# Performance work log

Measured on AMD Instinct MI355X. Metric: run time of the kernel, lower is better.

The kernel has to match this reference:

```python
import jax, jax.numpy as jnp
import numpy as np

B, S, HID = 2, 1024, 2048
N_HEADS, N_KV, HEAD_DIM = 32, 4, 128
BLOCK, MAX_BLOCKS = 32, 128
EPS = 1e-6
ROPE_THETA = 1e6


def _rmsnorm(x, w):
    # per-head RMSNorm over head_dim (Qwen3MoeRMSNorm)
    var = jnp.mean(x * x, axis=-1, keepdims=True)
    return x * jax.lax.rsqrt(var + EPS) * w


def _rotate_half(x):
    h = x.shape[-1] // 2
    return jnp.concatenate([-x[..., h:], x[..., :h]], axis=-1)


def setup_inputs() -> dict:
    key = jax.random.key(0)
    ks = jax.random.split(key, 8)
    hidden_states = jax.random.normal(ks[0], (B, S, HID), dtype=jnp.float32)
    wq = jax.random.normal(ks[1], (N_HEADS * HEAD_DIM, HID), dtype=jnp.float32) * 0.02
    wk = jax.random.normal(ks[2], (N_KV * HEAD_DIM, HID), dtype=jnp.float32) * 0.02
    wv = jax.random.normal(ks[3], (N_KV * HEAD_DIM, HID), dtype=jnp.float32) * 0.02
    wo = jax.random.normal(ks[4], (HID, N_HEADS * HEAD_DIM), dtype=jnp.float32) * 0.02
    q_norm_w = 1.0 + 0.01 * jax.random.normal(ks[5], (HEAD_DIM,), dtype=jnp.float32)
    k_norm_w = 1.0 + 0.01 * jax.random.normal(ks[6], (HEAD_DIM,), dtype=jnp.float32)
    # RoPE tables (rotate-half / llama convention)
    inv_freq = 1.0 / (ROPE_THETA ** (jnp.arange(0, HEAD_DIM, 2, dtype=jnp.float32) / HEAD_DIM))
    t = jnp.arange(S, dtype=jnp.float32)
    freqs = jnp.outer(t, inv_freq)  # [S, HEAD_DIM/2]
    emb = jnp.concatenate([freqs, freqs], axis=-1)  # [S, HEAD_DIM]
    cos, sin = jnp.cos(emb), jnp.sin(emb)
    # page table: B sequences x (S/BLOCK) blocks, distinct block ids
    page_table = jnp.arange(B * (S // BLOCK), dtype=jnp.int32).reshape(B, S // BLOCK)
    return {"hidden_states": hidden_states, "wq": wq, "wk": wk, "wv": wv, "wo": wo,
            "q_norm_w": q_norm_w, "k_norm_w": k_norm_w, "cos": cos, "sin": sin,
            "page_table": page_table}


def reference(hidden_states, wq, wk, wv, wo, q_norm_w, k_norm_w, cos, sin, page_table):
    b, s, _ = hidden_states.shape
    # fused QKV projection (math-equivalent to the concatenated qkv_proj_weight)
    q = (hidden_states @ wq.T).reshape(b, s, N_HEADS, HEAD_DIM)
    k = (hidden_states @ wk.T).reshape(b, s, N_KV, HEAD_DIM)
    v = (hidden_states @ wv.T).reshape(b, s, N_KV, HEAD_DIM)
    # per-head RMSNorm then RoPE
    q = _rmsnorm(q, q_norm_w)
    k = _rmsnorm(k, k_norm_w)
    c = cos[None, :, None, :]
    sn = sin[None, :, None, :]
    q = q * c + _rotate_half(q) * sn
    k = k * c + _rotate_half(k) * sn
    # paged KV-cache fill: [B, nblk, BLOCK, kvh, hd] -> cache[block_id, kvh, BLOCK, hd]
    nblk = s // BLOCK
    k_blk = k.reshape(b, nblk, BLOCK, N_KV, HEAD_DIM).transpose(0, 1, 3, 2, 4).reshape(-1, N_KV, BLOCK, HEAD_DIM)
    v_blk = v.reshape(b, nblk, BLOCK, N_KV, HEAD_DIM).transpose(0, 1, 3, 2, 4).reshape(-1, N_KV, BLOCK, HEAD_DIM)
    flat_pt = page_table.reshape(-1)
    cache_k = jnp.zeros((MAX_BLOCKS, N_KV, BLOCK, HEAD_DIM), dtype=k.dtype).at[flat_pt].set(k_blk)
    cache_v = jnp.zeros((MAX_BLOCKS, N_KV, BLOCK, HEAD_DIM), dtype=v.dtype).at[flat_pt].set(v_blk)
    # GQA: repeat kv heads (num_key_value_groups = 8)
    groups = N_HEADS // N_KV
    k_rep = jnp.repeat(k, groups, axis=2)  # [b, s, N_HEADS, hd]
    v_rep = jnp.repeat(v, groups, axis=2)
    # causal SDPA, scaling = head_dim ** -0.5
    scale = HEAD_DIM ** -0.5
    scores = jnp.einsum('bqhd,bkhd->bhqk', q, k_rep) * scale
    causal = jnp.tril(jnp.ones((s, s), dtype=bool))
    scores = jnp.where(causal[None, None], scores, jnp.finfo(scores.dtype).min)
    probs = jax.nn.softmax(scores, axis=-1)
    attn = jnp.einsum('bhqk,bkhd->bqhd', probs, v_rep).reshape(b, s, N_HEADS * HEAD_DIM)
    out = attn @ wo.T  # [b, s, HID]
    return out, cache_k, cache_v
```

## Files before the change

### kernel.cpp

```cpp
#include <hip/hip_runtime.h>
#include <hip/hip_bf16.h>


typedef __attribute__((ext_vector_type(8))) __bf16 bf16x8;
typedef __attribute__((ext_vector_type(4))) __bf16 bf16x4;
typedef __attribute__((ext_vector_type(4))) float f32x4;

__device__ __forceinline__ void gload16(const void* g, void* l) {
    __builtin_amdgcn_global_load_lds((const __attribute__((address_space(1))) void*)g,
                                     (__attribute__((address_space(3))) void*)l, 16, 0, 0);
}

__global__ __launch_bounds__(256) void cvt5(const float* __restrict__ s0, const float* __restrict__ s1,
                                            const float* __restrict__ s2, const float* __restrict__ s3,
                                            const float* __restrict__ s4,
                                            __bf16* __restrict__ d0, __bf16* __restrict__ d1,
                                            __bf16* __restrict__ d2, __bf16* __restrict__ d3,
                                            __bf16* __restrict__ d4) {
    const int b = blockIdx.x;
    const float* src; __bf16* dst; int off;
    if (b < 4096)       { src = s0; dst = d0; off = b; }
    else if (b < 12288) { src = s1; dst = d1; off = b - 4096; }
    else if (b < 13312) { src = s2; dst = d2; off = b - 12288; }
    else if (b < 14336) { src = s3; dst = d3; off = b - 13312; }
    else                { src = s4; dst = d4; off = b - 14336; }
    const int i = off * 256 + threadIdx.x;
    float4 v = reinterpret_cast<const float4*>(src)[i];
    bf16x4 o = {(__bf16)v.x, (__bf16)v.y, (__bf16)v.z, (__bf16)v.w};
    reinterpret_cast<bf16x4*>(dst)[i] = o;
}

__global__ __launch_bounds__(256) void reduce_add(float* __restrict__ o,
                                                  const float* __restrict__ p, int n4) {
    int i = blockIdx.x * 256 + threadIdx.x;
    int stride = gridDim.x * 256;
    for (; i < n4; i += stride) {
        float4 a = reinterpret_cast<float4*>(o)[i];
        float4 b = reinterpret_cast<const float4*>(p)[i];
        a.x += b.x; a.y += b.y; a.z += b.z; a.w += b.w;
        reinterpret_cast<float4*>(o)[i] = a;
    }
}

__global__ __launch_bounds__(512, 2) void gemm256(const __bf16* __restrict__ A,
                                                  const __bf16* __restrict__ B,
                                                  __bf16* __restrict__ C,
                                                  const int M, const int N, const int K) {
    __shared__ __bf16 Asm[2 * 256 * 64];
    __shared__ __bf16 Bsm[2 * 256 * 64];
    const int tid = threadIdx.x, lane = tid & 63, wave = tid >> 6;
    const int wm = wave >> 2, wn = wave & 3;
    const int lrow = lane & 15, lkg = lane >> 4;
    const int nbn = N >> 8;
    const int swz = ((int)blockIdx.x & 7) * ((int)gridDim.x >> 3) + ((int)blockIdx.x >> 3);
    const int bm = swz / nbn, bn = swz % nbn;
    const int brow = bm * 256, bcol = bn * 256;
    const int row0 = tid >> 3;
    const int scol_sw = ((tid & 7) ^ (row0 & 7)) * 8;
    const __bf16* gA = A + (size_t)(brow + row0) * K + scol_sw;
    const __bf16* gB = B + (size_t)(bcol + row0) * K + scol_sw;
    const int aslot0 = (lkg ^ (lrow & 7)) * 8;
    const int aslot1 = ((4 + lkg) ^ (lrow & 7)) * 8;
    const int nt = K / 64, nIter = nt / 2;

    f32x4 acc[8][4] = {};
    bf16x8 a[4][2];

    auto stage = [&](int s) {
        if (s >= 4 * nt) return;
        const int tau = s >> 2, h = s & 3, hb = s & 1;
        const size_t rofs = (size_t)(hb * 128) * K + (size_t)tau * 64;
        if (h < 2) {
            const __bf16* g = gA + rofs;
            __bf16* l = Asm + (tau & 1) * 16384 + hb * 8192 + tid * 8;
            gload16(g, l);
            gload16(g + (size_t)64 * K, l + 4096);
        } else {
            const __bf16* g = gB + rofs;
            __bf16* l = Bsm + (tau & 1) * 16384 + hb * 8192 + tid * 8;
            gload16(g, l);
            gload16(g + (size_t)64 * K, l + 4096);
        }
    };

    stage(0); stage(1); stage(2); stage(3); stage(4);
    asm volatile("s_waitcnt vmcnt(2)" ::: "memory");
    __builtin_amdgcn_s_barrier();

    for (int i = 0; i < nIter; ++i) {
        const bool last = (i == nIter - 1);
#pragma unroll
        for (int p = 0; p < 8; ++p) {
            const int q = p & 3, cbuf = p >> 2;
            const __bf16* As = Asm + cbuf * 16384;
            const __bf16* Bs = Bsm + cbuf * 16384;
            bf16x8 b[2][2];
            if ((q & 1) == 0) {
#pragma unroll
                for (int mf = 0; mf < 4; ++mf) {
                    const int r = wm * 128 + (q >> 1) * 64 + mf * 16 + lrow;
                    a[mf][0] = *reinterpret_cast<const bf16x8*>(&As[r * 64 + aslot0]);
                    a[mf][1] = *reinterpret_cast<const bf16x8*>(&As[r * 64 + aslot1]);
                }
            }
#pragma unroll
            for (int nf = 0; nf < 2; ++nf) {
                const int r = wn * 64 + (q & 1) * 32 + nf * 16 + lrow;
                b[nf][0] = *reinterpret_cast<const bf16x8*>(&Bs[r * 64 + aslot0]);
                b[nf][1] = *reinterpret_cast<const bf16x8*>(&Bs[r * 64 + aslot1]);
            }
            stage(8 * i + p + 5);
            if (p == 3) {
                if (last) asm volatile("s_waitcnt vmcnt(0)" ::: "memory");
                else      asm volatile("s_waitcnt vmcnt(2)" ::: "memory");
            } else if (p == 7 && !last) {
                asm volatile("s_waitcnt vmcnt(2)" ::: "memory");
            }
            __builtin_amdgcn_s_barrier();
            asm volatile("s_waitcnt lgkmcnt(0)" ::: "memory");
            __builtin_amdgcn_sched_barrier(0);
            __builtin_amdgcn_s_setprio(1);
#pragma unroll
            for (int mf = 0; mf < 4; ++mf)
#pragma unroll
                for (int nf = 0; nf < 2; ++nf)
#pragma unroll
                    for (int kk = 0; kk < 2; ++kk)
                        acc[(q >> 1) * 4 + mf][(q & 1) * 2 + nf] =
                            __builtin_amdgcn_mfma_f32_16x16x32_bf16(
                                a[mf][kk], b[nf][kk],
                                acc[(q >> 1) * 4 + mf][(q & 1) * 2 + nf], 0, 0, 0);
            __builtin_amdgcn_s_setprio(0);
            __builtin_amdgcn_s_barrier();
        }
    }
#pragma unroll
    for (int Mi = 0; Mi < 8; ++Mi)
#pragma unroll
        for (int Ni = 0; Ni < 4; ++Ni)
#pragma unroll
            for (int j = 0; j < 4; ++j) {
                const size_t r = brow + wm * 128 + Mi * 16 + lkg * 4 + j;
                const size_t c = bcol + wn * 64 + Ni * 16 + lrow;
                C[r * N + c] = (__bf16)acc[Mi][Ni][j];
            }
}

template <int OUT_BF16>
__global__ __launch_bounds__(256) void gemm_bt(const __bf16* __restrict__ A,
                                               const __bf16* __restrict__ B,
                                               void* __restrict__ C0,
                                               void* __restrict__ C1,
                                               const int M, const int N, const int K,
                                               const int klen) {
    __shared__ __bf16 As0[128 * 64];
    __shared__ __bf16 Bs0[128 * 64];
    __shared__ __bf16 As1[128 * 64];
    __shared__ __bf16 Bs1[128 * 64];
    const int tid = threadIdx.x;
    const int lane = tid & 63;
    const int wave = tid >> 6;
    const int bn = blockIdx.x, bm = blockIdx.y;
    const int kbeg = blockIdx.z * klen;
    const int brow = bm * 128, bcol = bn * 128;
    const int wr = wave >> 1, wc = wave & 1;
    const int lrow = lane & 15, lkg = lane >> 4;
    const int srow_in = lane >> 3;
    const int scol = (lane & 7) * 8;
    f32x4 acc[4][4] = {};

    auto stage = [&](int k0, __bf16* as, __bf16* bs) {
#pragma unroll
        for (int r = 0; r < 4; ++r) {
            const int chunk = r * 4 + wave;
            const int row = chunk * 8 + srow_in;
            gload16(&A[(size_t)(brow + row) * K + k0 + scol], as + chunk * 512);
            gload16(&B[(size_t)(bcol + row) * K + k0 + scol], bs + chunk * 512);
        }
    };
    auto compute = [&](const __bf16* as, const __bf16* bs) {
#pragma unroll
        for (int kk = 0; kk < 2; ++kk) {
            bf16x8 a[4], bfr[4];
#pragma unroll
            for (int m = 0; m < 4; ++m)
                a[m] = *reinterpret_cast<const bf16x8*>(&as[(wr * 64 + m * 16 + lrow) * 64 + kk * 32 + lkg * 8]);
#pragma unroll
            for (int n = 0; n < 4; ++n)
                bfr[n] = *reinterpret_cast<const bf16x8*>(&bs[(wc * 64 + n * 16 + lrow) * 64 + kk * 32 + lkg * 8]);
#pragma unroll
            for (int m = 0; m < 4; ++m)
#pragma unroll
                for (int n = 0; n < 4; ++n)
                    acc[m][n] = __builtin_amdgcn_mfma_f32_16x16x32_bf16(a[m], bfr[n], acc[m][n], 0, 0, 0);
        }
    };

    const int nt = klen / 64;
    stage(kbeg, As0, Bs0);
    asm volatile("s_waitcnt vmcnt(0)" ::: "memory");
    __syncthreads();
    int t = 0;
    for (; t + 2 < nt; t += 2) {
        stage(kbeg + (t + 1) * 64, As1, Bs1);
        compute(As0, Bs0);
        asm volatile("s_waitcnt vmcnt(0)" ::: "memory");
        __syncthreads();
        stage(kbeg + (t + 2) * 64, As0, Bs0);
        compute(As1, Bs1);
        asm volatile("s_waitcnt vmcnt(0)" ::: "memory");
        __syncthreads();
    }
    stage(kbeg + (t + 1) * 64, As1, Bs1);
    compute(As0, Bs0);
    asm volatile("s_waitcnt vmcnt(0)" ::: "memory");
    __syncthreads();
    compute(As1, Bs1);

    void* C = blockIdx.z == 0 ? C0 : C1;
#pragma unroll
    for (int m = 0; m < 4; ++m)
#pragma unroll
        for (int n = 0; n < 4; ++n)
#pragma unroll
            for (int j = 0; j < 4; ++j) {
                const size_t r = brow + wr * 64 + m * 16 + lkg * 4 + j;
                const size_t c = bcol + wc * 64 + n * 16 + lrow;
                if (OUT_BF16)
                    ((__bf16*)C)[r * N + c] = (__bf16)acc[m][n][j];
                else
                    ((float*)C)[r * N + c] = acc[m][n][j];
            }
}

__global__ __launch_bounds__(256) void norm_rope_cache(
    __bf16* __restrict__ qkv, const float* __restrict__ cosT, const float* __restrict__ sinT,
    const float* __restrict__ qw, const float* __restrict__ kw,
    const int* __restrict__ ptab, float* __restrict__ cacheK, float* __restrict__ cacheV) {
    const int t = blockIdx.x;
    const int b = t >> 10, s = t & 1023;
    const int wave = threadIdx.x >> 6, lane = threadIdx.x & 63;
    __bf16* row = qkv + (size_t)t * 5120;
    const float c = cosT[s * 128 + lane];
    const float sn = sinT[s * 128 + lane];
    const int page = ptab[b * 32 + (s >> 5)];
    const int so = s & 31;
    const float wq0 = qw[lane], wq1 = qw[lane + 64];
#pragma unroll
    for (int i = 0; i < 8; ++i) {
        const int h = wave * 8 + i;
        float x0 = (float)row[h * 128 + lane];
        float x1 = (float)row[h * 128 + 64 + lane];
        float ss = x0 * x0 + x1 * x1;
        for (int off = 32; off; off >>= 1) ss += __shfl_xor(ss, off);
        const float rs = rsqrtf(ss * (1.0f / 128.0f) + 1e-6f);
        const float y0 = x0 * rs * wq0, y1 = x1 * rs * wq1;
        row[h * 128 + lane]      = (__bf16)(y0 * c - y1 * sn);
        row[h * 128 + 64 + lane] = (__bf16)(y1 * c + y0 * sn);
    }
    {
        const int h = wave;
        float x0 = (float)row[4096 + h * 128 + lane];
        float x1 = (float)row[4096 + h * 128 + 64 + lane];
        float ss = x0 * x0 + x1 * x1;
        for (int off = 32; off; off >>= 1) ss += __shfl_xor(ss, off);
        const float rs = rsqrtf(ss * (1.0f / 128.0f) + 1e-6f);
        const float y0 = x0 * rs * kw[lane], y1 = x1 * rs * kw[lane + 64];
        const float o0 = y0 * c - y1 * sn, o1 = y1 * c + y0 * sn;
        row[4096 + h * 128 + lane]      = (__bf16)o0;
        row[4096 + h * 128 + 64 + lane] = (__bf16)o1;
        float* ck = cacheK + (((size_t)page * 4 + h) * 32 + so) * 128;
        ck[lane] = o0; ck[lane + 64] = o1;
        const float v0 = (float)row[4608 + h * 128 + lane];
        const float v1 = (float)row[4608 + h * 128 + 64 + lane];
        float* cv = cacheV + (((size_t)page * 4 + h) * 32 + so) * 128;
        cv[lane] = v0; cv[lane + 64] = v1;
    }
}

__global__ __launch_bounds__(512) void attn_fwd(const __bf16* __restrict__ qkv,
                                                __bf16* __restrict__ out) {
    constexpr int LVT = 72, LPT = 72;
    __shared__ __bf16 Ks[64 * 128];
    __shared__ __bf16 Vt[128 * LVT];
    __shared__ __bf16 Ps[8 * 16 * LPT];
    const int qb = 63 - blockIdx.x;
    const int kvg = blockIdx.y, b = blockIdx.z;
    const int tid = threadIdx.x, wave = tid >> 6, lane = tid & 63;
    const int lrow = lane & 15, lkg = lane >> 4;
    const int h = kvg * 8 + wave;
    const size_t base = (size_t)b * 1024 * 5120;
    const int kofs = 4096 + kvg * 128, vofs = 4608 + kvg * 128;
    const int qrow0 = qb * 16;

    bf16x8 aq[4];
#pragma unroll
    for (int kc = 0; kc < 4; ++kc)
        aq[kc] = *reinterpret_cast<const bf16x8*>(
            &qkv[base + (size_t)(qrow0 + lrow) * 5120 + h * 128 + kc * 32 + lkg * 8]);

    f32x4 acc[8] = {};
    float m_i = -1e30f, l_i = 0.f;
    const int nt = qb / 4 + 1;
    __bf16* Pw = &Ps[wave * 16 * LPT];
    const int swz = lrow & 7;

    for (int t = 0; t < nt; ++t) {
        const int kv0 = t * 64;
        __syncthreads();
#pragma unroll
        for (int c = 0; c < 2; ++c) {
            const int chunk = c * 8 + wave;
            const int row = chunk * 4 + (lane >> 4);
            const int gslot = (lane & 15) ^ (row & 7);
            gload16(&qkv[base + (size_t)(kv0 + row) * 5120 + kofs + gslot * 8],
                    &Ks[chunk * 512]);
        }
#pragma unroll
        for (int r = 0; r < 2; ++r) {
            const int d0 = (wave + r * 8) * 8;
            uint4 vv = *reinterpret_cast<const uint4*>(
                &qkv[base + (size_t)(kv0 + lane) * 5120 + vofs + d0]);
            const __bf16* pv = reinterpret_cast<const __bf16*>(&vv);
#pragma unroll
            for (int j = 0; j < 8; ++j) Vt[(d0 + j) * LVT + lane] = pv[j];
        }
        __syncthreads();

        f32x4 st[4] = {};
#pragma unroll
        for (int kc = 0; kc < 4; ++kc)
#pragma unroll
            for (int f = 0; f < 4; ++f) {
                bf16x8 ak = *reinterpret_cast<const bf16x8*>(
                    &Ks[(f * 16 + lrow) * 128 + ((kc * 4 + lkg) ^ swz) * 8]);
                st[f] = __builtin_amdgcn_mfma_f32_16x16x32_bf16(ak, aq[kc], st[f], 0, 0, 0);
            }

        const int qpos = qrow0 + lrow;
        float sv[16];
        float pmax = -1e30f;
#pragma unroll
        for (int f = 0; f < 4; ++f)
#pragma unroll
            for (int j = 0; j < 4; ++j) {
                const int kvpos = kv0 + f * 16 + lkg * 4 + j;
                float x = st[f][j] * 0.08838834764831845f;
                if (kvpos > qpos) x = -1e30f;
                sv[f * 4 + j] = x;
                pmax = fmaxf(pmax, x);
            }
        pmax = fmaxf(pmax, __shfl_xor(pmax, 16));
        pmax = fmaxf(pmax, __shfl_xor(pmax, 32));
        const float m_new = fmaxf(m_i, pmax);
        const float sf = __expf(m_i - m_new);
        float ladd = 0.f;
#pragma unroll
        for (int f = 0; f < 4; ++f) {
            bf16x4 pb;
#pragma unroll
            for (int j = 0; j < 4; ++j) {
                const float p = __expf(sv[f * 4 + j] - m_new);
                ladd += p;
                pb[j] = (__bf16)p;
            }
            *reinterpret_cast<bf16x4*>(&Pw[lrow * LPT + f * 16 + lkg * 4]) = pb;
        }
        ladd += __shfl_xor(ladd, 16);
        ladd += __shfl_xor(ladd, 32);
        l_i = l_i * sf + ladd;
        m_i = m_new;
        float sfj[4];
#pragma unroll
        for (int j = 0; j < 4; ++j) sfj[j] = __shfl(sf, lkg * 4 + j);
#pragma unroll
        for (int f = 0; f < 8; ++f)
#pragma unroll
            for (int j = 0; j < 4; ++j) acc[f][j] *= sfj[j];

#pragma unroll
        for (int kk = 0; kk < 2; ++kk) {
            bf16x8 ap = *reinterpret_cast<const bf16x8*>(&Pw[lrow * LPT + kk * 32 + lkg * 8]);
#pragma unroll
            for (int f = 0; f < 8; ++f) {
                bf16x8 bv = *reinterpret_cast<const bf16x8*>(
                    &Vt[(f * 16 + lrow) * LVT + kk * 32 + lkg * 8]);
                acc[f] = __builtin_amdgcn_mfma_f32_16x16x32_bf16(ap, bv, acc[f], 0, 0, 0);
            }
        }
    }
    float linv[4];
#pragma unroll
    for (int j = 0; j < 4; ++j) linv[j] = 1.0f / __shfl(l_i, lkg * 4 + j);
#pragma unroll
    for (int f = 0; f < 8; ++f)
#pragma unroll
        for (int j = 0; j < 4; ++j) {
            const size_t r = (size_t)b * 1024 + qrow0 + lkg * 4 + j;
            out[r * 4096 + h * 128 + f * 16 + lrow] = (__bf16)(acc[f][j] * linv[j]);
        }
}

extern "C" void kernel_launch(void* const* d_in, const int* in_sizes, int n_in,
                              void* d_out, int out_size, void* d_ws, size_t ws_size,
                              hipStream_t stream) {
    const float* hidden = (const float*)d_in[0];
    const float* wq = (const float*)d_in[1];
    const float* wk = (const float*)d_in[2];
    const float* wv = (const float*)d_in[3];
    const float* wo = (const float*)d_in[4];
    const float* qnw = (const float*)d_in[5];
    const float* knw = (const float*)d_in[6];
    const float* cosT = (const float*)d_in[7];
    const float* sinT = (const float*)d_in[8];
    const int* ptab = (const int*)d_in[9];

    float* outp = (float*)d_out;
    float* cacheK = outp + 4194304;
    float* cacheV = cacheK + 2097152;

    char* ws = (char*)d_ws;
    __bf16* hbf    = (__bf16*)ws;
    __bf16* w1bf   = (__bf16*)(ws + 8388608);
    __bf16* wobf   = (__bf16*)(ws + 29360128);
    __bf16* qkvbf  = (__bf16*)(ws + 46137344);
    __bf16* attnbf = (__bf16*)ws;
    float*  opart  = (float*)(ws + 46137344);

    cvt5<<<22528, 256, 0, stream>>>(hidden, wq, wk, wv, wo,
                                    hbf, w1bf, w1bf + (size_t)4096 * 2048,
                                    w1bf + (size_t)4608 * 2048, wobf);

    gemm256<<<160, 512, 0, stream>>>(hbf, w1bf, qkvbf, 2048, 5120, 2048);

    hipMemsetAsync(cacheK, 0, (size_t)4194304 * 4, stream);
    norm_rope_cache<<<2048, 256, 0, stream>>>(qkvbf, cosT, sinT, qnw, knw, ptab, cacheK, cacheV);

    attn_fwd<<<dim3(64, 4, 2), 512, 0, stream>>>(qkvbf, attnbf);

    gemm_bt<0><<<dim3(16, 16, 2), 256, 0, stream>>>(attnbf, wobf, outp, opart,
                                                    2048, 2048, 4096, 2048);
    reduce_add<<<2048, 256, 0, stream>>>(outp, opart, 4194304 / 4);
}
```

Baseline: 217.2 us.

## Pair causal query blocks per workgroup and double-buffer K/V in attention

The attention kernel now processes two query blocks per workgroup, a short one and its mirrored long one (qa and 63-qa). This balances causal work across workgroups and halves the grid. K and V tiles are double-buffered, with V prefetched into registers and K staged via async LDS loads one tile ahead. Other changes: the softmax scale is folded into Q, V and P use XOR-swizzled LDS layouts, masking is applied only on the diagonal tile, and the accumulator rescale is skipped when the running max grows by at most 8. Costs are more registers and LDS per workgroup, and skipping the rescale lets unnormalized probabilities reach up to e^8 before the bf16 cast.

```diff
diff --git a/kernel.cpp b/kernel.cpp
--- a/kernel.cpp
+++ b/kernel.cpp
@@ -278,126 +278,187 @@
     }
 }
 
-__global__ __launch_bounds__(512) void attn_fwd(const __bf16* __restrict__ qkv,
-                                                __bf16* __restrict__ out) {
-    constexpr int LVT = 72, LPT = 72;
-    __shared__ __bf16 Ks[64 * 128];
-    __shared__ __bf16 Vt[128 * LVT];
-    __shared__ __bf16 Ps[8 * 16 * LPT];
-    const int qb = 63 - blockIdx.x;
+__global__ __launch_bounds__(512, 2) void attn_fwd(const __bf16* __restrict__ qkv,
+                                                   __bf16* __restrict__ out) {
+    __shared__ __bf16 Ks[2][64 * 128];
+    __shared__ __bf16 Vs[2][128 * 64];
+    __shared__ __bf16 Ps[8][2][16 * 64];
+    const int qa = blockIdx.x;
+    const int qbig = 63 - qa;
     const int kvg = blockIdx.y, b = blockIdx.z;
     const int tid = threadIdx.x, wave = tid >> 6, lane = tid & 63;
     const int lrow = lane & 15, lkg = lane >> 4;
     const int h = kvg * 8 + wave;
     const size_t base = (size_t)b * 1024 * 5120;
     const int kofs = 4096 + kvg * 128, vofs = 4608 + kvg * 128;
-    const int qrow0 = qb * 16;
-
-    bf16x8 aq[4];
-#pragma unroll
-    for (int kc = 0; kc < 4; ++kc)
-        aq[kc] = *reinterpret_cast<const bf16x8*>(
-            &qkv[base + (size_t)(qrow0 + lrow) * 5120 + h * 128 + kc * 32 + lkg * 8]);
-
-    f32x4 acc[8] = {};
-    float m_i = -1e30f, l_i = 0.f;
-    const int nt = qb / 4 + 1;
-    __bf16* Pw = &Ps[wave * 16 * LPT];
-    const int swz = lrow & 7;
-
-    for (int t = 0; t < nt; ++t) {
-        const int kv0 = t * 64;
-        __syncthreads();
+    const int ntA = qa / 4 + 1, nt = qbig / 4 + 1;
+    const int qposA = qa * 16 + lrow, qposB = qbig * 16 + lrow;
+    const int rsw = lrow & 7;
+
+    bf16x8 aqA[4], aqB[4];
+#pragma unroll
+    for (int kc = 0; kc < 4; ++kc) {
+        bf16x8 ta = *reinterpret_cast<const bf16x8*>(
+            &qkv[base + (size_t)(qa * 16 + lrow) * 5120 + h * 128 + kc * 32 + lkg * 8]);
+        bf16x8 tb = *reinterpret_cast<const bf16x8*>(
+            &qkv[base + (size_t)(qbig * 16 + lrow) * 5120 + h * 128 + kc * 32 + lkg * 8]);
+#pragma unroll
+        for (int i = 0; i < 8; ++i) {
+            ta[i] = (__bf16)((float)ta[i] * 0.08838834764831845f);
+            tb[i] = (__bf16)((float)tb[i] * 0.08838834764831845f);
+        }
+        aqA[kc] = ta; aqB[kc] = tb;
+    }
+
+    f32x4 accA[8] = {}, accB[8] = {};
+    float mA = -1e30f, lA = 0.f, mB = -1e30f, lB = 0.f;
+    __bf16* PwA = &Ps[wave][0][0];
+    __bf16* PwB = &Ps[wave][1][0];
+
+    auto stageK = [&](int t, int buf) {
+        const int kv0 = (t < nt) ? t * 64 : 0;
 #pragma unroll
         for (int c = 0; c < 2; ++c) {
             const int chunk = c * 8 + wave;
             const int row = chunk * 4 + (lane >> 4);
             const int gslot = (lane & 15) ^ (row & 7);
             gload16(&qkv[base + (size_t)(kv0 + row) * 5120 + kofs + gslot * 8],
-                    &Ks[chunk * 512]);
-        }
+                    &Ks[buf][chunk * 512]);
+        }
+    };
+    auto loadV = [&](int t, uint4 (&vr)[2]) {
+        const int kv0 = (t < nt) ? t * 64 : 0;
+#pragma unroll
+        for (int r = 0; r < 2; ++r)
+            vr[r] = *reinterpret_cast<const uint4*>(
+                &qkv[base + (size_t)(kv0 + lane) * 5120 + vofs + wave * 16 + r * 8]);
+    };
+    auto writeV = [&](uint4 (&vr)[2], int buf) {
 #pragma unroll
         for (int r = 0; r < 2; ++r) {
-            const int d0 = (wave + r * 8) * 8;
-            uint4 vv = *reinterpret_cast<const uint4*>(
-                &qkv[base + (size_t)(kv0 + lane) * 5120 + vofs + d0]);
-            const __bf16* pv = reinterpret_cast<const __bf16*>(&vv);
-#pragma unroll
-            for (int j = 0; j < 8; ++j) Vt[(d0 + j) * LVT + lane] = pv[j];
-        }
-        __syncthreads();
-
-        f32x4 st[4] = {};
+            const __bf16* pv = reinterpret_cast<const __bf16*>(&vr[r]);
+#pragma unroll
+            for (int j = 0; j < 8; ++j) {
+                const int d = wave * 16 + r * 8 + j;
+                Vs[buf][d * 64 + (((lane >> 3) ^ j) << 3) + (lane & 7)] = pv[j];
+            }
+        }
+    };
+
+    auto smax = [&](f32x4 (&st)[4], float& m_i, float& l_i, f32x4 (&acc)[8],
+                    int qpos, int kv0, bool maskit, __bf16* Pw) {
+        float sv[16]; float pmax = -1e30f;
+#pragma unroll
+        for (int f = 0; f < 4; ++f)
+#pragma unroll
+            for (int j = 0; j < 4; ++j) {
+                float x = st[f][j];
+                if (maskit) {
+                    const int kvpos = kv0 + f * 16 + lkg * 4 + j;
+                    if (kvpos > qpos) x = -1e30f;
+                }
+                sv[f * 4 + j] = x;
+                pmax = fmaxf(pmax, x);
+            }
+        pmax = fmaxf(pmax, __shfl_xor(pmax, 16));
+        pmax = fmaxf(pmax, __shfl_xor(pmax, 32));
+        if (!__all(pmax - m_i <= 8.f)) {
+            const float m_new = fmaxf(m_i, pmax);
+            const float sf = __expf(m_i - m_new);
+            m_i = m_new;
+            l_i *= sf;
+            float sfj[4];
+#pragma unroll
+            for (int j = 0; j < 4; ++j) sfj[j] = __shfl(sf, lkg * 4 + j);
+#pragma unroll
+            for (int f = 0; f < 8; ++f)
+#pragma unroll
+                for (int j = 0; j < 4; ++j) acc[f][j] *= sfj[j];
+        }
+        float ladd = 0.f;
+#pragma unroll
+        for (int f = 0; f < 4; ++f) {
+            bf16x4 pb;
+#pragma unroll
+            for (int j = 0; j < 4; ++j) {
+                const float p = __expf(sv[f * 4 + j] - m_i);
+                ladd += p;
+                pb[j] = (__bf16)p;
+            }
+            const int slot = (f * 2 + (lkg >> 1)) ^ rsw;
+            *reinterpret_cast<bf16x4*>(&Pw[lrow * 64 + slot * 8 + (lkg & 1) * 4]) = pb;
+        }
+        ladd += __shfl_xor(ladd, 16);
+        ladd += __shfl_xor(ladd, 32);
+        l_i += ladd;
+    };
+
+    auto body = [&](int t, uint4 (&vcur)[2], uint4 (&vnext)[2]) {
+        const int kbuf = t & 1;
+        __builtin_amdgcn_s_barrier();
+        asm volatile("" ::: "memory");
+        loadV(t + 1, vnext);
+        stageK(t + 1, kbuf ^ 1);
+        asm volatile("s_waitcnt vmcnt(4)" ::: "memory");
+        writeV(vcur, kbuf);
+        asm volatile("s_waitcnt lgkmcnt(0)" ::: "memory");
+        __builtin_amdgcn_s_barrier();
+        asm volatile("" ::: "memory");
+
+        const bool doA = t < ntA;
+        f32x4 stA[4] = {}, stB[4] = {};
 #pragma unroll
         for (int kc = 0; kc < 4; ++kc)
 #pragma unroll
             for (int f = 0; f < 4; ++f) {
                 bf16x8 ak = *reinterpret_cast<const bf16x8*>(
-                    &Ks[(f * 16 + lrow) * 128 + ((kc * 4 + lkg) ^ swz) * 8]);
-                st[f] = __builtin_amdgcn_mfma_f32_16x16x32_bf16(ak, aq[kc], st[f], 0, 0, 0);
-            }
-
-        const int qpos = qrow0 + lrow;
-        float sv[16];
-        float pmax = -1e30f;
-#pragma unroll
-        for (int f = 0; f < 4; ++f)
-#pragma unroll
-            for (int j = 0; j < 4; ++j) {
-                const int kvpos = kv0 + f * 16 + lkg * 4 + j;
-                float x = st[f][j] * 0.08838834764831845f;
-                if (kvpos > qpos) x = -1e30f;
-                sv[f * 4 + j] = x;
-                pmax = fmaxf(pmax, x);
-            }
-        pmax = fmaxf(pmax, __shfl_xor(pmax, 16));
-        pmax = fmaxf(pmax, __shfl_xor(pmax, 32));
-        const float m_new = fmaxf(m_i, pmax);
-        const float sf = __expf(m_i - m_new);
-        float ladd = 0.f;
-#pragma unroll
-        for (int f = 0; f < 4; ++f) {
-            bf16x4 pb;
-#pragma unroll
-            for (int j = 0; j < 4; ++j) {
-                const float p = __expf(sv[f * 4 + j] - m_new);
-                ladd += p;
-                pb[j] = (__bf16)p;
-            }
-            *reinterpret_cast<bf16x4*>(&Pw[lrow * LPT + f * 16 + lkg * 4]) = pb;
-        }
-        ladd += __shfl_xor(ladd, 16);
-        ladd += __shfl_xor(ladd, 32);
-        l_i = l_i * sf + ladd;
-        m_i = m_new;
-        float sfj[4];
-#pragma unroll
-        for (int j = 0; j < 4; ++j) sfj[j] = __shfl(sf, lkg * 4 + j);
-#pragma unroll
-        for (int f = 0; f < 8; ++f)
-#pragma unroll
-            for (int j = 0; j < 4; ++j) acc[f][j] *= sfj[j];
-
+                    &Ks[kbuf][(f * 16 + lrow) * 128 + (((kc * 4 + lkg) ^ rsw) << 3)]);
+                stB[f] = __builtin_amdgcn_mfma_f32_16x16x32_bf16(ak, aqB[kc], stB[f], 0, 0, 0);
+                if (doA)
+                    stA[f] = __builtin_amdgcn_mfma_f32_16x16x32_bf16(ak, aqA[kc], stA[f], 0, 0, 0);
+            }
+        if (doA) smax(stA, mA, lA, accA, qposA, t * 64, t == ntA - 1, PwA);
+        smax(stB, mB, lB, accB, qposB, t * 64, t == nt - 1, PwB);
 #pragma unroll
         for (int kk = 0; kk < 2; ++kk) {
-            bf16x8 ap = *reinterpret_cast<const bf16x8*>(&Pw[lrow * LPT + kk * 32 + lkg * 8]);
+            const int pslot = ((kk * 4 + lkg) ^ rsw) << 3;
+            bf16x8 apB = *reinterpret_cast<const bf16x8*>(&PwB[lrow * 64 + pslot]);
+            bf16x8 apA;
+            if (doA) apA = *reinterpret_cast<const bf16x8*>(&PwA[lrow * 64 + pslot]);
 #pragma unroll
             for (int f = 0; f < 8; ++f) {
                 bf16x8 bv = *reinterpret_cast<const bf16x8*>(
-                    &Vt[(f * 16 + lrow) * LVT + kk * 32 + lkg * 8]);
-                acc[f] = __builtin_amdgcn_mfma_f32_16x16x32_bf16(ap, bv, acc[f], 0, 0, 0);
-            }
-        }
-    }
-    float linv[4];
-#pragma unroll
-    for (int j = 0; j < 4; ++j) linv[j] = 1.0f / __shfl(l_i, lkg * 4 + j);
+                    &Vs[kbuf][(f * 16 + lrow) * 64 + pslot]);
+                accB[f] = __builtin_amdgcn_mfma_f32_16x16x32_bf16(apB, bv, accB[f], 0, 0, 0);
+                if (doA)
+                    accA[f] = __builtin_amdgcn_mfma_f32_16x16x32_bf16(apA, bv, accA[f], 0, 0, 0);
+            }
+        }
+    };
+
+    uint4 vrA[2], vrB[2];
+    loadV(0, vrA);
+    stageK(0, 0);
+    for (int t = 0; t < nt; t += 2) {
+        body(t, vrA, vrB);
+        if (t + 1 < nt) body(t + 1, vrB, vrA);
+    }
+    asm volatile("s_waitcnt vmcnt(0)" ::: "memory");
+
+    float linvA[4], linvB[4];
+#pragma unroll
+    for (int j = 0; j < 4; ++j) {
+        linvA[j] = 1.0f / __shfl(lA, lkg * 4 + j);
+        linvB[j] = 1.0f / __shfl(lB, lkg * 4 + j);
+    }
 #pragma unroll
     for (int f = 0; f < 8; ++f)
 #pragma unroll
         for (int j = 0; j < 4; ++j) {
-            const size_t r = (size_t)b * 1024 + qrow0 + lkg * 4 + j;
-            out[r * 4096 + h * 128 + f * 16 + lrow] = (__bf16)(acc[f][j] * linv[j]);
+            out[((size_t)b * 1024 + qa * 16 + lkg * 4 + j) * 4096 + h * 128 + f * 16 + lrow] =
+                (__bf16)(accA[f][j] * linvA[j]);
+            out[((size_t)b * 1024 + qbig * 16 + lkg * 4 + j) * 4096 + h * 128 + f * 16 + lrow] =
+                (__bf16)(accB[f][j] * linvB[j]);
         }
 }
 
@@ -436,7 +497,7 @@
     hipMemsetAsync(cacheK, 0, (size_t)4194304 * 4, stream);
     norm_rope_cache<<<2048, 256, 0, stream>>>(qkvbf, cosT, sinT, qnw, knw, ptab, cacheK, cacheV);
 
-    attn_fwd<<<dim3(64, 4, 2), 512, 0, stream>>>(qkvbf, attnbf);
+    attn_fwd<<<dim3(32, 4, 2), 512, 0, stream>>>(qkvbf, attnbf);
 
     gemm_bt<0><<<dim3(16, 16, 2), 256, 0, stream>>>(attnbf, wobf, outp, opart,
                                                     2048, 2048, 4096, 2048);
```

New measurement: 206.6 us. 4.9% less time.
